# Kernel tuning notes

Hardware: AMD Instinct MI355X
Metric: run time of the kernel (lower is better)

## Reference

```python
import jax, jax.numpy as jnp
import numpy as np

M = 81920          # total triples = 1024 groups * (2*39 + 2)
NB = 39            # num_neighbor
TOTAL_ENT = 14541
TOTAL_REL = 237
D = 100            # embedding_dim == BiLSTM_input_size
H = 100            # lstm hidden (== hidden_size1)
ALPHA = 0.2
MU = 0.001


def _lstm_seq(x, Wih, Whh, b):
    """x: [B,T,D] -> hidden states [B,T,H]. PyTorch gate order i,f,g,o."""
    B = x.shape[0]
    Hh = Whh.shape[1]
    def step(carry, xt):
        h, c = carry
        g = xt @ Wih.T + h @ Whh.T + b
        i, f, gg, o = jnp.split(g, 4, axis=-1)
        c = jax.nn.sigmoid(f) * c + jax.nn.sigmoid(i) * jnp.tanh(gg)
        h = jax.nn.sigmoid(o) * jnp.tanh(c)
        return (h, c), h
    init = (jnp.zeros((B, Hh), x.dtype), jnp.zeros((B, Hh), x.dtype))
    _, hs = jax.lax.scan(step, init, jnp.swapaxes(x, 0, 1))
    return jnp.swapaxes(hs, 0, 1)


def _gat(inp, W, a_vec):
    """inp: [B,N,F] -> [B,F]. GAT-style attention against node 0, thresholded by MU."""
    h = jnp.einsum('bnf,fo->bno', inp, W)
    a0 = jnp.broadcast_to(h[:, :1, :], h.shape)           # node-0 features repeated
    e = jax.nn.leaky_relu(jnp.concatenate([h, a0], axis=-1) @ a_vec, ALPHA)  # [B,N,1]
    att = jax.nn.softmax(e, axis=1)
    att = jnp.maximum(att - MU, 0.0)                      # (x + |x|)/2 == relu(x)
    return jnp.einsum('bnl,bnf->bf', att, h)              # l == 1


def setup_inputs():
    key = jax.random.key(0)
    ks = jax.random.split(key, 20)
    u = 6.0 / np.sqrt(D)        # embedding uniform range as in the module
    sl = 1.0 / np.sqrt(H)       # pytorch LSTM init scale
    F6 = 6 * H
    def uni(k, shape, s):
        return jax.random.uniform(k, shape, minval=-s, maxval=s, dtype=jnp.float32)
    xav1 = 1.414 * np.sqrt(2.0 / (F6 + F6))
    xav2 = 1.414 * np.sqrt(2.0 / (H + H))
    return {
        'batch_h': jax.random.randint(ks[0], (M,), 0, TOTAL_ENT),
        'batch_r': jax.random.randint(ks[1], (M,), 0, TOTAL_REL),
        'batch_t': jax.random.randint(ks[2], (M,), 0, TOTAL_ENT),
        'ent_emb': uni(ks[3], (TOTAL_ENT, D), u),
        'rel_emb': uni(ks[4], (TOTAL_REL, D), u),
        'ent_emb1': uni(ks[5], (TOTAL_ENT, D), u),
        'rel_emb1': uni(ks[6], (TOTAL_REL, D), u),
        'Wih_f': uni(ks[7], (4 * H, D), sl),
        'Whh_f': uni(ks[8], (4 * H, H), sl),
        'b_f': uni(ks[9], (4 * H,), sl),
        'Wih_b': uni(ks[10], (4 * H, D), sl),
        'Whh_b': uni(ks[11], (4 * H, H), sl),
        'b_b': uni(ks[12], (4 * H,), sl),
        'Wih_p': uni(ks[13], (4 * H, D), sl),
        'Whh_p': uni(ks[14], (4 * H, H), sl),
        'b_p': uni(ks[15], (4 * H,), sl),
        'W_att1': jax.random.normal(ks[16], (F6, F6), dtype=jnp.float32) * xav1,
        'a_att1': jax.random.normal(ks[17], (2 * F6, 1), dtype=jnp.float32) * 0.05,
        'W_att2': jax.random.normal(ks[18], (H, H), dtype=jnp.float32) * xav2,
        'a_att2': jax.random.normal(ks[19], (2 * H, 1), dtype=jnp.float32) * 0.05,
    }


def reference(batch_h, batch_r, batch_t, ent_emb, rel_emb, ent_emb1, rel_emb1,
              Wih_f, Whh_f, b_f, Wih_b, Whh_b, b_b, Wih_p, Whh_p, b_p,
              W_att1, a_att1, W_att2, a_att2):
    # triple -> [M,3,D] sequence (head, relation, tail)
    x = jnp.stack([ent_emb[batch_h], rel_emb[batch_r], ent_emb[batch_t]], axis=1)
    # bidirectional LSTM (num_layers=1), zero init states
    of = _lstm_seq(x, Wih_f, Whh_f, b_f)
    ob = _lstm_seq(x[:, ::-1], Wih_b, Whh_b, b_b)[:, ::-1]
    out = jnp.concatenate([of, ob], axis=-1).reshape(x.shape[0], -1)   # [M, 6H]
    out_att = _gat(out.reshape(-1, NB + 1, 6 * H), W_att1, a_att1)     # [M/40, 6H]
    out2 = out.reshape(-1, 2 * NB + 2, 6 * H)                          # [M/80, 80, 6H]
    # second branch: unidirectional ProcessLSTM, last timestep (fc is unused in torch code)
    x1 = jnp.stack([ent_emb1[batch_h], rel_emb1[batch_r], ent_emb1[batch_t]], axis=1)
    op = _lstm_seq(x1, Wih_p, Whh_p, b_p)[:, -1, :]                    # [M, H]
    output_att = _gat(op.reshape(-1, NB + 1, H), W_att2, a_att2)       # [M/40, H]
    op2 = op.reshape(-1, 2 * NB + 2, H)
    return out2[:, 0, :], out_att, op2[:, 0, :], output_att
```

## Files before the change

kernel.cpp:

```cpp
#include <hip/hip_runtime.h>
#include <hip/hip_bf16.h>
#include <cstdint>
#include <cstddef>
#include <cmath>

#define TID ((int)threadIdx.x)

typedef __attribute__((ext_vector_type(8))) short bf16x8;
typedef __attribute__((ext_vector_type(4))) float f32x4;
typedef __attribute__((ext_vector_type(4))) unsigned short us4;
typedef unsigned short ushort_t;

__device__ __forceinline__ float bfu2f(unsigned short u){
    unsigned int x = ((unsigned int)u) << 16; float f; __builtin_memcpy(&f, &x, 4); return f;
}
__device__ __forceinline__ unsigned short f2bu(float f){
    __hip_bfloat16 b = __float2bfloat16(f); unsigned short u; __builtin_memcpy(&u, &b, 2); return u;
}
__device__ __forceinline__ float sigm(float x){
    return __builtin_amdgcn_rcpf(1.0f + __expf(-x));
}
__device__ __forceinline__ float tanhx(float x){
    return 1.0f - 2.0f*__builtin_amdgcn_rcpf(1.0f + __expf(2.0f*x));
}
__device__ __forceinline__ void bar_lds(){ asm volatile("s_waitcnt lgkmcnt(0)\n\ts_barrier" ::: "memory"); }

__global__ __launch_bounds__(256) void k_prep(
    const float* __restrict__ Wih_f, const float* __restrict__ Wih_b, const float* __restrict__ Wih_p,
    const float* __restrict__ Whh_f, const float* __restrict__ Whh_b, const float* __restrict__ Whh_p,
    const float* __restrict__ b_f, const float* __restrict__ b_b, const float* __restrict__ b_p,
    const float* __restrict__ W1, const float* __restrict__ a1,
    const float* __restrict__ W2, const float* __restrict__ a2,
    unsigned short* __restrict__ Asw3, unsigned short* __restrict__ Wsw3,
    float* __restrict__ bI3,
    float* __restrict__ w1a, float* __restrict__ w1b,
    float* __restrict__ w2a, float* __restrict__ w2b)
{
    int bx = blockIdx.x;
    if (bx < 1200){
        int isW = (bx >= 600) ? 1 : 0;
        int e = (bx - isW*600)*256 + TID;
        int l = e/51200, r = e - l*51200;
        int frag = r >> 9, q = r & 511;
        int lanep = q >> 3, j = q & 7;
        int mt = frag >> 2, kt = frag & 3;
        int m = mt*16 + (lanep & 15);
        int f = m >> 2, gg = m & 3;
        int k = kt*32 + (lanep >> 4)*8 + j;
        const float* Ws = isW ? ((l==0)?Wih_f:(l==1)?Wih_b:Wih_p)
                              : ((l==0)?Whh_f:(l==1)?Whh_b:Whh_p);
        float v = (k < 100) ? Ws[(gg*100+f)*100 + k] : 0.f;
        (isW ? Wsw3 : Asw3)[e] = f2bu(v);
    } else if (bx == 1200){
        for (int e=TID; e<1200; e+=256){
            int l = e/400, m = e - l*400;
            int f = m >> 2, gg = m & 3;
            const float* bb = (l==0)?b_f:(l==1)?b_b:b_p;
            bI3[e] = bb[gg*100+f];
        }
    } else {
        int lane = TID & 63, w = TID >> 6;
        int r = (bx - 1201)*4 + w;
        if (r < 600){
            float x=0.f, y=0.f;
            for (int k=lane;k<600;k+=64){ float wv=W1[r*600+k]; x+=wv*a1[k]; y+=wv*a1[600+k]; }
#pragma unroll
            for (int off=32;off>0;off>>=1){ x+=__shfl_down(x,off,64); y+=__shfl_down(y,off,64); }
            if (lane==0){ w1a[r]=x; w1b[r]=y; }
        } else if (r < 700){
            int f = r-600;
            float x=0.f, y=0.f;
            for (int k=lane;k<100;k+=64){ float wv=W2[f*100+k]; x+=wv*a2[k]; y+=wv*a2[100+k]; }
#pragma unroll
            for (int off=32;off>0;off>>=1){ x+=__shfl_down(x,off,64); y+=__shfl_down(y,off,64); }
            if (lane==0){ w2a[f]=x; w2b[f]=y; }
        }
    }
}

__global__ __launch_bounds__(256) void k_projm(
    const float* __restrict__ ent, const float* __restrict__ rel,
    const float* __restrict__ ent1, const float* __restrict__ rel1,
    const unsigned short* __restrict__ Wsw3, const float* __restrict__ bI3,
    unsigned short* __restrict__ Pfe, unsigned short* __restrict__ Pfr,
    unsigned short* __restrict__ Pbe, unsigned short* __restrict__ Pbr,
    unsigned short* __restrict__ Ppe, unsigned short* __restrict__ Ppr)
{
    int y = blockIdx.y;
    int l = y >> 1;
    int isrel = y & 1;
    int rows = isrel ? 237 : 14541;
    int r0 = blockIdx.x * 64;
    if (r0 >= rows) return;
    const float* emb  = isrel ? ((l==2)? rel1 : rel) : ((l==2)? ent1 : ent);
    unsigned short* P = (y==0)?Pfe:(y==1)?Pfr:(y==2)?Pbe:(y==3)?Pbr:(y==4)?Ppe:Ppr;
    const unsigned short* A = Wsw3 + l*51200;
    const float* bI = bI3 + l*400;

    __shared__ __align__(16) ushort_t EB[64][136];
    for (int idx=TID; idx<64*128; idx+=256){
        int r = idx >> 7, k = idx & 127;
        int rg = r0 + r;
        float v = (rg < rows && k < 100) ? emb[rg*100 + k] : 0.f;
        EB[r][k] = f2bu(v);
    }
    __syncthreads();

    int lane = TID & 63, w = TID >> 6, l15 = lane & 15, quad = lane >> 4;
    int rg = r0 + w*16 + l15;
    bf16x8 bfr[4];
#pragma unroll
    for (int kt=0;kt<4;kt++) bfr[kt] = *(const bf16x8*)&EB[w*16 + l15][kt*32 + quad*8];

    for (int mt=0; mt<25; mt++){
        f32x4 acc = (f32x4){0.f,0.f,0.f,0.f};
#pragma unroll
        for (int kt=0;kt<4;kt++){
            bf16x8 af = *(const bf16x8*)(A + ((mt*4+kt)*64 + lane)*8);
            acc = __builtin_amdgcn_mfma_f32_16x16x32_bf16(af, bfr[kt], acc, 0, 0, 0);
        }
        f32x4 bv = *(const f32x4*)(bI + mt*16 + quad*4);
        us4 o;
#pragma unroll
        for (int r=0;r<4;r++) o[r] = f2bu(acc[r] + bv[r]);
        if (rg < rows) *(us4*)(P + (size_t)rg*400 + mt*16 + quad*4) = o;
    }
}

__global__ __launch_bounds__(256, 2) void k_fused(
    const int* __restrict__ bh, const int* __restrict__ br, const int* __restrict__ bt,
    const unsigned short* __restrict__ Pfe, const unsigned short* __restrict__ Pfr,
    const unsigned short* __restrict__ Pbe, const unsigned short* __restrict__ Pbr,
    const unsigned short* __restrict__ Ppe, const unsigned short* __restrict__ Ppr,
    const unsigned short* __restrict__ Asw3,
    const float* __restrict__ w1a, const float* __restrict__ w1b,
    const float* __restrict__ w2a, const float* __restrict__ w2b,
    float* __restrict__ z, float* __restrict__ z2,
    float* __restrict__ out0, float* __restrict__ op0)
{
    __shared__ __align__(16) ushort_t HA[48][136];
    __shared__ __align__(16) ushort_t HO[40][600];
    __shared__ float sc1[40], tc1[40], sc2[40], tc2[40];
    __shared__ float att1[40], att2[40];
    __shared__ int sidx[3][40];

    int g = blockIdx.x;
    int m0 = g*40;
    if (TID < 40){
        sidx[0][TID] = bh[m0+TID];
        sidx[1][TID] = br[m0+TID];
        sidx[2][TID] = bt[m0+TID];
    }
    for (int i=TID; i<48*136; i+=256) ((ushort_t*)HA)[i] = 0;
    __syncthreads();

    int lane = TID & 63;
    int wid  = TID >> 6;
    int l15  = lane & 15;
    int quad = lane >> 4;
    int nmt  = (wid==0) ? 7 : 6;
    bool doS0 = ((g & 1) == 0);
    int rrow = g >> 1;
    int s2i = (l15 < 8) ? (32 + l15) : 0;

    const unsigned short* PeA[3] = {Pfe, Pbe, Ppe};
    const unsigned short* PrA[3] = {Pfr, Pbr, Ppr};

    float c[21];
    us4 pv[7][3];

    {
        int e0 = sidx[0][l15], e1 = sidx[0][16+l15], e2 = sidx[0][s2i];
#pragma unroll
        for (int i=0;i<7;i++){
            if (i < nmt){
                int f4 = ((wid + 4*i)*4 + quad)*4;
                pv[i][0] = *(const us4*)(Pfe + (size_t)e0*400 + f4);
                pv[i][1] = *(const us4*)(Pfe + (size_t)e1*400 + f4);
                pv[i][2] = *(const us4*)(Pfe + (size_t)e2*400 + f4);
            }
        }
    }

    for (int l=0; l<3; l++){
        const unsigned short* Aswl = Asw3 + l*51200;
        for (int t=0; t<3; t++){
            bf16x8 bfr[3][4];
            if (t > 0){
#pragma unroll
                for (int nt=0;nt<3;nt++)
#pragma unroll
                    for (int kt=0;kt<4;kt++)
                        bfr[nt][kt] = *(const bf16x8*)&HA[nt*16 + l15][kt*32 + quad*8];
                bar_lds();
            }

            int wslotbase = (l==0) ? t*200 : (2-t)*200 + 100;
#pragma unroll
            for (int i=0;i<7;i++){
                if (i < nmt){
                    f32x4 acc3[3];
#pragma unroll
                    for (int nt=0;nt<3;nt++) acc3[nt] = (f32x4){0.f,0.f,0.f,0.f};
                    if (t > 0){
                        int mt = wid + 4*i;
#pragma unroll
                        for (int kt=0;kt<4;kt++){
                            bf16x8 af = *(const bf16x8*)(Aswl + ((mt*4+kt)*64 + lane)*8);
#pragma unroll
                            for (int nt=0;nt<3;nt++)
                                acc3[nt] = __builtin_amdgcn_mfma_f32_16x16x32_bf16(
                                    af, bfr[nt][kt], acc3[nt], 0, 0, 0);
                        }
                    }
                    int f = (wid + 4*i)*4 + quad;
#pragma unroll
                    for (int nt=0;nt<3;nt++){
                        int s = nt*16 + l15;
                        bool valid = (nt < 2) || (l15 < 8);
                        us4 p4 = pv[i][nt];
                        f32x4 a4 = acc3[nt];
                        float gi = a4[0] + bfu2f(p4[0]);
                        float gf = a4[1] + bfu2f(p4[1]);
                        float gg = a4[2] + bfu2f(p4[2]);
                        float go = a4[3] + bfu2f(p4[3]);
                        float cp = (t==0) ? 0.f : c[i*3+nt];
                        float cn = sigm(gf)*cp + sigm(gi)*tanhx(gg);
                        float h  = sigm(go)*tanhx(cn);
                        c[i*3+nt] = cn;
                        if (valid){
                            if (t < 2 || l == 2) HA[s][f] = f2bu(h);
                            if (l < 2){
                                int slot = wslotbase + f;
                                HO[s][slot] = f2bu(h);
                                if (doS0 && s==0) out0[(size_t)rrow*600 + slot] = h;
                            } else if (t==2 && doS0 && s==0){
                                op0[(size_t)rrow*100 + f] = h;
                            }
                        }
                    }
                }
            }

            if (!(l==2 && t==2)){
                int ln = (t==2) ? l+1 : l;
                int tn = (t==2) ? 0 : t+1;
                int pn = (ln==1) ? (2-tn) : tn;
                const unsigned short* tabn = (pn==1) ? PrA[ln] : PeA[ln];
                int e0 = sidx[pn][l15], e1 = sidx[pn][16+l15], e2 = sidx[pn][s2i];
#pragma unroll
                for (int i=0;i<7;i++){
                    if (i < nmt){
                        int f4 = ((wid + 4*i)*4 + quad)*4;
                        pv[i][0] = *(const us4*)(tabn + (size_t)e0*400 + f4);
                        pv[i][1] = *(const us4*)(tabn + (size_t)e1*400 + f4);
                        pv[i][2] = *(const us4*)(tabn + (size_t)e2*400 + f4);
                    }
                }
            }

            bar_lds();
        }
    }

    for (int n = wid; n < 40; n += 4){
        float a=0.f, b=0.f;
        for (int k=lane;k<600;k+=64){ float v=bfu2f(HO[n][k]); a += v*w1a[k]; b += v*w1b[k]; }
#pragma unroll
        for (int off=32; off>0; off>>=1){ a += __shfl_down(a,off,64); b += __shfl_down(b,off,64); }
        if (lane==0){ sc1[n]=a; tc1[n]=b; }
        float a2=0.f, b2=0.f;
        for (int k=lane;k<100;k+=64){ float v=bfu2f(HA[n][k]); a2 += v*w2a[k]; b2 += v*w2b[k]; }
#pragma unroll
        for (int off=32; off>0; off>>=1){ a2 += __shfl_down(a2,off,64); b2 += __shfl_down(b2,off,64); }
        if (lane==0){ sc2[n]=a2; tc2[n]=b2; }
    }
    __syncthreads();

    if (wid < 2){
        const float* sc = (wid==0)? sc1 : sc2;
        const float* tc = (wid==0)? tc1 : tc2;
        float* av       = (wid==0)? att1 : att2;
        float e = -1e30f;
        if (lane < 40){
            float x = sc[lane] + tc[0];
            e = (x > 0.f) ? x : 0.2f*x;
        }
        float mx = e;
#pragma unroll
        for (int off=32;off>0;off>>=1) mx = fmaxf(mx, __shfl_down(mx,off,64));
        mx = __shfl(mx, 0, 64);
        float pexp = (lane<40) ? __expf(e-mx) : 0.f;
        float sm = pexp;
#pragma unroll
        for (int off=32;off>0;off>>=1) sm += __shfl_down(sm,off,64);
        sm = __shfl(sm, 0, 64);
        if (lane < 40){
            float a = pexp/sm - 0.001f;
            av[lane] = (a > 0.f) ? a : 0.f;
        }
    }
    __syncthreads();

    for (int j=TID; j<600; j+=256){
        float acc = 0.f;
#pragma unroll
        for (int n=0;n<40;n++) acc += att1[n]*bfu2f(HO[n][j]);
        z[(size_t)g*600 + j] = acc;
    }
    for (int j=TID; j<100; j+=256){
        float acc = 0.f;
#pragma unroll
        for (int n=0;n<40;n++) acc += att2[n]*bfu2f(HA[n][j]);
        z2[(size_t)g*100 + j] = acc;
    }
}

__global__ __launch_bounds__(256) void k_post(const float* __restrict__ z, const float* __restrict__ z2,
    const float* __restrict__ W1, const float* __restrict__ W2,
    float* __restrict__ oatt, float* __restrict__ oatt2)
{
    extern __shared__ float zl[];
    int y = blockIdx.y;
    const float* zz = (y==3)? z2 : z;
    const float* W  = (y==3)? W2 : W1;
    float* o        = (y==3)? oatt2 : oatt;
    int dim         = (y==3)? 100 : 600;
    int rb = blockIdx.x*16;
    for (int r=0;r<16;r++){
        for (int j=TID;j<dim;j+=256) zl[r*dim+j] = zz[(size_t)(rb+r)*dim + j];
    }
    __syncthreads();
    int cc = (y==3)? TID : y*256 + TID;
    if (cc < dim){
        float acc[16];
#pragma unroll
        for (int r=0;r<16;r++) acc[r]=0.f;
        for (int k=0;k<dim;k++){
            float w = W[(size_t)k*dim + cc];
#pragma unroll
            for (int r=0;r<16;r++) acc[r] += zl[r*dim+k]*w;
        }
        for (int r=0;r<16;r++) o[(size_t)(rb+r)*dim + cc] = acc[r];
    }
}

__global__ void k_sentinel(float* o, float v){ o[0] = v; }

extern "C" void kernel_launch(void* const* d_in, const int* in_sizes, int n_in,
                              void* d_out, int out_size, void* d_ws, size_t ws_size,
                              hipStream_t stream)
{
    const int*   bh   = (const int*)d_in[0];
    const int*   br   = (const int*)d_in[1];
    const int*   bt   = (const int*)d_in[2];
    const float* ent  = (const float*)d_in[3];
    const float* rel  = (const float*)d_in[4];
    const float* ent1 = (const float*)d_in[5];
    const float* rel1 = (const float*)d_in[6];
    const float* Wih_f = (const float*)d_in[7];
    const float* Whh_f = (const float*)d_in[8];
    const float* b_f   = (const float*)d_in[9];
    const float* Wih_b = (const float*)d_in[10];
    const float* Whh_b = (const float*)d_in[11];
    const float* b_b   = (const float*)d_in[12];
    const float* Wih_p = (const float*)d_in[13];
    const float* Whh_p = (const float*)d_in[14];
    const float* b_p   = (const float*)d_in[15];
    const float* W1 = (const float*)d_in[16];
    const float* a1 = (const float*)d_in[17];
    const float* W2 = (const float*)d_in[18];
    const float* a2 = (const float*)d_in[19];

    char* wsb = (char*)d_ws;
    size_t off = 0;
    auto alloc = [&](size_t bytes) -> char* {
        char* p = wsb + off;
        off += (bytes + 255) & ~(size_t)255;
        return p;
    };
    unsigned short* Pfe = (unsigned short*)alloc((size_t)14541*400*2);
    unsigned short* Pbe = (unsigned short*)alloc((size_t)14541*400*2);
    unsigned short* Ppe = (unsigned short*)alloc((size_t)14541*400*2);
    unsigned short* Pfr = (unsigned short*)alloc((size_t)237*400*2);
    unsigned short* Pbr = (unsigned short*)alloc((size_t)237*400*2);
    unsigned short* Ppr = (unsigned short*)alloc((size_t)237*400*2);
    unsigned short* Asw3 = (unsigned short*)alloc((size_t)153600*2);
    unsigned short* Wsw3 = (unsigned short*)alloc((size_t)153600*2);
    float* bI3 = (float*)alloc(1200*4);
    float* w1a = (float*)alloc(600*4);
    float* w1b = (float*)alloc(600*4);
    float* w2a = (float*)alloc(100*4);
    float* w2b = (float*)alloc(100*4);
    float* z   = (float*)alloc((size_t)2048*600*4);
    float* z2  = (float*)alloc((size_t)2048*100*4);

    float* dout  = (float*)d_out;
    float* out0  = dout;
    float* oatt  = dout + 614400;
    float* op0   = dout + 1843200;
    float* oatt2 = dout + 1945600;

    if (ws_size < off){
        k_sentinel<<<1,1,0,stream>>>(dout, (float)ws_size);
        return;
    }

    k_prep<<<1376, 256, 0, stream>>>(Wih_f, Wih_b, Wih_p, Whh_f, Whh_b, Whh_p,
                                     b_f, b_b, b_p, W1, a1, W2, a2,
                                     Asw3, Wsw3, bI3, w1a, w1b, w2a, w2b);

    k_projm<<<dim3(228,6), 256, 0, stream>>>(ent, rel, ent1, rel1, Wsw3, bI3,
                                             Pfe, Pfr, Pbe, Pbr, Ppe, Ppr);

    k_fused<<<2048, 256, 0, stream>>>(bh, br, bt, Pfe, Pfr, Pbe, Pbr, Ppe, Ppr,
                                      Asw3, w1a, w1b, w2a, w2b, z, z2, out0, op0);

    k_post<<<dim3(128,4), 256, 16*600*4, stream>>>(z, z2, W1, W2, oatt, oatt2);
}
```

Measured before the change: 594.2 us.

## Split fused LSTM/GAT kernel to cut LDS use and stage gate gathers in LDS

Splits the fused kernel into an LSTM kernel and a separate attention kernel for the 600-wide branch. The LSTM kernel no longer keeps the full 40x600 hidden buffer in LDS. Instead it streams each step's hidden states to a global bf16 buffer, and it gathers projected gate rows into an LDS staging tile rather than prefetching them into registers. This lowers LDS and register pressure so three blocks can run per CU. The cost is an extra ~98MB global write and read round trip, an additional launch, and the loss of the register prefetch overlap.

```diff
diff --git a/kernel.cpp b/kernel.cpp
--- a/kernel.cpp
+++ b/kernel.cpp
@@ -23,7 +23,6 @@
 __device__ __forceinline__ float tanhx(float x){
     return 1.0f - 2.0f*__builtin_amdgcn_rcpf(1.0f + __expf(2.0f*x));
 }
-__device__ __forceinline__ void bar_lds(){ asm volatile("s_waitcnt lgkmcnt(0)\n\ts_barrier" ::: "memory"); }
 
 __global__ __launch_bounds__(256) void k_prep(
     const float* __restrict__ Wih_f, const float* __restrict__ Wih_b, const float* __restrict__ Wih_p,
@@ -127,31 +126,33 @@
     }
 }
 
-__global__ __launch_bounds__(256, 2) void k_fused(
+__global__ __launch_bounds__(256, 3) void k_lstm(
     const int* __restrict__ bh, const int* __restrict__ br, const int* __restrict__ bt,
     const unsigned short* __restrict__ Pfe, const unsigned short* __restrict__ Pfr,
     const unsigned short* __restrict__ Pbe, const unsigned short* __restrict__ Pbr,
     const unsigned short* __restrict__ Ppe, const unsigned short* __restrict__ Ppr,
     const unsigned short* __restrict__ Asw3,
-    const float* __restrict__ w1a, const float* __restrict__ w1b,
     const float* __restrict__ w2a, const float* __restrict__ w2b,
-    float* __restrict__ z, float* __restrict__ z2,
+    unsigned short* __restrict__ out, float* __restrict__ z2,
     float* __restrict__ out0, float* __restrict__ op0)
 {
+    __shared__ __align__(16) ushort_t Pst[40][408];
     __shared__ __align__(16) ushort_t HA[48][136];
-    __shared__ __align__(16) ushort_t HO[40][600];
-    __shared__ float sc1[40], tc1[40], sc2[40], tc2[40];
-    __shared__ float att1[40], att2[40];
+    __shared__ float S0o[600];
+    __shared__ float S0p[100];
+    __shared__ float sc2[40], tc2[40], att2[40];
     __shared__ int sidx[3][40];
 
-    int g = blockIdx.x;
-    int m0 = g*40;
+    int g = blockIdx.x, m0 = g*40;
     if (TID < 40){
         sidx[0][TID] = bh[m0+TID];
         sidx[1][TID] = br[m0+TID];
         sidx[2][TID] = bt[m0+TID];
     }
-    for (int i=TID; i<48*136; i+=256) ((ushort_t*)HA)[i] = 0;
+    {
+        us4 zz; zz[0]=0; zz[1]=0; zz[2]=0; zz[3]=0;
+        for (int i=TID; i<1632; i+=256) ((us4*)HA)[i] = zz;
+    }
     __syncthreads();
 
     int lane = TID & 63;
@@ -161,30 +162,31 @@
     int nmt  = (wid==0) ? 7 : 6;
     bool doS0 = ((g & 1) == 0);
     int rrow = g >> 1;
-    int s2i = (l15 < 8) ? (32 + l15) : 0;
 
     const unsigned short* PeA[3] = {Pfe, Pbe, Ppe};
     const unsigned short* PrA[3] = {Pfr, Pbr, Ppr};
 
     float c[21];
-    us4 pv[7][3];
-
-    {
-        int e0 = sidx[0][l15], e1 = sidx[0][16+l15], e2 = sidx[0][s2i];
-#pragma unroll
-        for (int i=0;i<7;i++){
-            if (i < nmt){
-                int f4 = ((wid + 4*i)*4 + quad)*4;
-                pv[i][0] = *(const us4*)(Pfe + (size_t)e0*400 + f4);
-                pv[i][1] = *(const us4*)(Pfe + (size_t)e1*400 + f4);
-                pv[i][2] = *(const us4*)(Pfe + (size_t)e2*400 + f4);
-            }
-        }
-    }
+    int prevbase = -1;
 
     for (int l=0; l<3; l++){
         const unsigned short* Aswl = Asw3 + l*51200;
         for (int t=0; t<3; t++){
+            int p = (l==1) ? (2-t) : t;
+            const unsigned short* tab = (p==1) ? PrA[l] : PeA[l];
+
+            if (prevbase >= 0){
+                for (int idx=TID; idx<1000; idx+=256){
+                    int s = idx/25, ch = idx - s*25;
+                    *(us4*)(out + (size_t)(m0+s)*600 + prevbase + ch*4) =
+                        *(const us4*)&HA[s][ch*4];
+                }
+            }
+            for (int idx=TID; idx<2000; idx+=256){
+                int s = idx/50, ch = idx - s*50;
+                *(bf16x8*)&Pst[s][ch*8] =
+                    *(const bf16x8*)(tab + (size_t)sidx[p][s]*400 + ch*8);
+            }
             bf16x8 bfr[3][4];
             if (t > 0){
 #pragma unroll
@@ -192,10 +194,10 @@
 #pragma unroll
                     for (int kt=0;kt<4;kt++)
                         bfr[nt][kt] = *(const bf16x8*)&HA[nt*16 + l15][kt*32 + quad*8];
-                bar_lds();
             }
-
-            int wslotbase = (l==0) ? t*200 : (2-t)*200 + 100;
+            __syncthreads();
+
+            int wbase = (l==0) ? t*200 : (l==1) ? (2-t)*200 + 100 : 0;
 #pragma unroll
             for (int i=0;i<7;i++){
                 if (i < nmt){
@@ -218,7 +220,8 @@
                     for (int nt=0;nt<3;nt++){
                         int s = nt*16 + l15;
                         bool valid = (nt < 2) || (l15 < 8);
-                        us4 p4 = pv[i][nt];
+                        int sr = valid ? s : 0;
+                        us4 p4 = *(const us4*)&Pst[sr][f*4];
                         f32x4 a4 = acc3[nt];
                         float gi = a4[0] + bfu2f(p4[0]);
                         float gf = a4[1] + bfu2f(p4[1]);
@@ -229,46 +232,21 @@
                         float h  = sigm(go)*tanhx(cn);
                         c[i*3+nt] = cn;
                         if (valid){
-                            if (t < 2 || l == 2) HA[s][f] = f2bu(h);
-                            if (l < 2){
-                                int slot = wslotbase + f;
-                                HO[s][slot] = f2bu(h);
-                                if (doS0 && s==0) out0[(size_t)rrow*600 + slot] = h;
-                            } else if (t==2 && doS0 && s==0){
-                                op0[(size_t)rrow*100 + f] = h;
+                            HA[s][f] = f2bu(h);
+                            if (doS0 && s==0){
+                                if (l < 2)            S0o[wbase + f] = h;
+                                else if (t == 2)      S0p[f] = h;
                             }
                         }
                     }
                 }
             }
-
-            if (!(l==2 && t==2)){
-                int ln = (t==2) ? l+1 : l;
-                int tn = (t==2) ? 0 : t+1;
-                int pn = (ln==1) ? (2-tn) : tn;
-                const unsigned short* tabn = (pn==1) ? PrA[ln] : PeA[ln];
-                int e0 = sidx[pn][l15], e1 = sidx[pn][16+l15], e2 = sidx[pn][s2i];
-#pragma unroll
-                for (int i=0;i<7;i++){
-                    if (i < nmt){
-                        int f4 = ((wid + 4*i)*4 + quad)*4;
-                        pv[i][0] = *(const us4*)(tabn + (size_t)e0*400 + f4);
-                        pv[i][1] = *(const us4*)(tabn + (size_t)e1*400 + f4);
-                        pv[i][2] = *(const us4*)(tabn + (size_t)e2*400 + f4);
-                    }
-                }
-            }
-
-            bar_lds();
+            prevbase = (l==2) ? -1 : wbase;
+            __syncthreads();
         }
     }
 
     for (int n = wid; n < 40; n += 4){
-        float a=0.f, b=0.f;
-        for (int k=lane;k<600;k+=64){ float v=bfu2f(HO[n][k]); a += v*w1a[k]; b += v*w1b[k]; }
-#pragma unroll
-        for (int off=32; off>0; off>>=1){ a += __shfl_down(a,off,64); b += __shfl_down(b,off,64); }
-        if (lane==0){ sc1[n]=a; tc1[n]=b; }
         float a2=0.f, b2=0.f;
         for (int k=lane;k<100;k+=64){ float v=bfu2f(HA[n][k]); a2 += v*w2a[k]; b2 += v*w2b[k]; }
 #pragma unroll
@@ -276,14 +254,10 @@
         if (lane==0){ sc2[n]=a2; tc2[n]=b2; }
     }
     __syncthreads();
-
-    if (wid < 2){
-        const float* sc = (wid==0)? sc1 : sc2;
-        const float* tc = (wid==0)? tc1 : tc2;
-        float* av       = (wid==0)? att1 : att2;
+    if (wid == 0){
         float e = -1e30f;
         if (lane < 40){
-            float x = sc[lane] + tc[0];
+            float x = sc2[lane] + tc2[0];
             e = (x > 0.f) ? x : 0.2f*x;
         }
         float mx = e;
@@ -297,22 +271,68 @@
         sm = __shfl(sm, 0, 64);
         if (lane < 40){
             float a = pexp/sm - 0.001f;
-            av[lane] = (a > 0.f) ? a : 0.f;
-        }
-    }
-    __syncthreads();
-
+            att2[lane] = (a > 0.f) ? a : 0.f;
+        }
+    }
+    __syncthreads();
+    for (int j=TID; j<100; j+=256){
+        float acc = 0.f;
+#pragma unroll
+        for (int n=0;n<40;n++) acc += att2[n]*bfu2f(HA[n][j]);
+        z2[(size_t)g*100 + j] = acc;
+    }
+    if (doS0){
+        for (int j=TID; j<600; j+=256) out0[(size_t)rrow*600 + j] = S0o[j];
+        for (int j=TID; j<100; j+=256) op0[(size_t)rrow*100 + j] = S0p[j];
+    }
+}
+
+__global__ __launch_bounds__(256, 3) void k_att(const unsigned short* __restrict__ out,
+    const float* __restrict__ w1a, const float* __restrict__ w1b, float* __restrict__ z)
+{
+    __shared__ __align__(16) ushort_t RL[40][600];
+    __shared__ float sc1[40], tc1[40], att1[40];
+    int g = blockIdx.x, m0 = g*40;
+    for (int idx=TID; idx<3000; idx+=256){
+        int n = idx/75, ch = idx - n*75;
+        *(bf16x8*)&RL[n][ch*8] = *(const bf16x8*)(out + (size_t)(m0+n)*600 + ch*8);
+    }
+    __syncthreads();
+    int lane = TID & 63, wid = TID >> 6;
+    for (int n = wid; n < 40; n += 4){
+        float a=0.f, b=0.f;
+        for (int k=lane;k<600;k+=64){ float v=bfu2f(RL[n][k]); a += v*w1a[k]; b += v*w1b[k]; }
+#pragma unroll
+        for (int off=32; off>0; off>>=1){ a += __shfl_down(a,off,64); b += __shfl_down(b,off,64); }
+        if (lane==0){ sc1[n]=a; tc1[n]=b; }
+    }
+    __syncthreads();
+    if (wid == 0){
+        float e = -1e30f;
+        if (lane < 40){
+            float x = sc1[lane] + tc1[0];
+            e = (x > 0.f) ? x : 0.2f*x;
+        }
+        float mx = e;
+#pragma unroll
+        for (int off=32;off>0;off>>=1) mx = fmaxf(mx, __shfl_down(mx,off,64));
+        mx = __shfl(mx, 0, 64);
+        float pexp = (lane<40) ? __expf(e-mx) : 0.f;
+        float sm = pexp;
+#pragma unroll
+        for (int off=32;off>0;off>>=1) sm += __shfl_down(sm,off,64);
+        sm = __shfl(sm, 0, 64);
+        if (lane < 40){
+            float a = pexp/sm - 0.001f;
+            att1[lane] = (a > 0.f) ? a : 0.f;
+        }
+    }
+    __syncthreads();
     for (int j=TID; j<600; j+=256){
         float acc = 0.f;
 #pragma unroll
-        for (int n=0;n<40;n++) acc += att1[n]*bfu2f(HO[n][j]);
+        for (int n=0;n<40;n++) acc += att1[n]*bfu2f(RL[n][j]);
         z[(size_t)g*600 + j] = acc;
-    }
-    for (int j=TID; j<100; j+=256){
-        float acc = 0.f;
-#pragma unroll
-        for (int n=0;n<40;n++) acc += att2[n]*bfu2f(HA[n][j]);
-        z2[(size_t)g*100 + j] = acc;
     }
 }
 
@@ -394,6 +414,7 @@
     float* w2b = (float*)alloc(100*4);
     float* z   = (float*)alloc((size_t)2048*600*4);
     float* z2  = (float*)alloc((size_t)2048*100*4);
+    unsigned short* outH = (unsigned short*)alloc((size_t)81920*600*2);
 
     float* dout  = (float*)d_out;
     float* out0  = dout;
@@ -413,8 +434,10 @@
     k_projm<<<dim3(228,6), 256, 0, stream>>>(ent, rel, ent1, rel1, Wsw3, bI3,
                                              Pfe, Pfr, Pbe, Pbr, Ppe, Ppr);
 
-    k_fused<<<2048, 256, 0, stream>>>(bh, br, bt, Pfe, Pfr, Pbe, Pbr, Ppe, Ppr,
-                                      Asw3, w1a, w1b, w2a, w2b, z, z2, out0, op0);
+    k_lstm<<<2048, 256, 0, stream>>>(bh, br, bt, Pfe, Pfr, Pbe, Pbr, Ppe, Ppr,
+                                     Asw3, w2a, w2b, outH, z2, out0, op0);
+
+    k_att<<<2048, 256, 0, stream>>>(outH, w1a, w1b, z);
 
     k_post<<<dim3(128,4), 256, 16*600*4, stream>>>(z, z2, W1, W2, oatt, oatt2);
 }
```

New measurement: 640.2 us. 1.08x slower.
